# Optimization experiments

Hardware: AMD Instinct MI355X
Metric: run time of the kernel (lower is better)

## Reference

```python
import jax, jax.numpy as jnp
import numpy as np

N_ENT = 100000
N_REL = 200  # directed relations = 2*N_REL
DIM = 200
N_EDGE = 1000000


def rotate(h, r):
    # complex 'rotate' composition: split last dim into (real, imag) halves
    d = h.shape[-1] // 2
    h_re, h_im = h[..., :d], h[..., d:]
    r_re, r_im = r[..., :d], r[..., d:]
    return jnp.concatenate([h_re * r_re - h_im * r_im,
                            h_re * r_im + h_im * r_re], axis=-1)


def setup_inputs() -> dict:
    key = jax.random.key(0)
    ks = jax.random.split(key, 8)
    return {
        "ent_emb": jax.random.normal(ks[0], (N_ENT, DIM), jnp.float32),
        "rel_emb": jax.random.normal(ks[1], (2 * N_REL, DIM), jnp.float32),
        "loop_rel": jax.random.normal(ks[2], (1, DIM), jnp.float32),
        "w_in": jax.random.normal(ks[3], (DIM, DIM), jnp.float32) * (DIM ** -0.5),
        "w_out": jax.random.normal(ks[4], (DIM, DIM), jnp.float32) * (DIM ** -0.5),
        "w_loop": jax.random.normal(ks[5], (DIM, DIM), jnp.float32) * (DIM ** -0.5),
        "bias": jnp.zeros((DIM,), jnp.float32),
        "bn_gamma": jnp.ones((DIM,), jnp.float32),
        "bn_beta": jnp.zeros((DIM,), jnp.float32),
        "edge_index": jax.random.randint(ks[6], (2, N_EDGE), 0, N_ENT, jnp.int64 if jax.config.jax_enable_x64 else jnp.int32),
        "edge_type": jax.random.randint(ks[7], (N_EDGE,), 0, N_REL, jnp.int64 if jax.config.jax_enable_x64 else jnp.int32),
    }


def reference(ent_emb, rel_emb, loop_rel, w_in, w_out, w_loop, bias,
              bn_gamma, bn_beta, edge_index, edge_type):
    n = ent_emb.shape[0]
    num_rel = rel_emb.shape[0] // 2
    src, dst = edge_index[0], edge_index[1]

    def direction(s, d, etype, W):
        # gather -> compose -> transform: [E, DIM]
        msg = rotate(ent_emb[s], rel_emb[etype]) @ W
        # symmetric degree normalization (CompGCN compute_norm)
        deg = jax.ops.segment_sum(jnp.ones_like(s, ent_emb.dtype), d, num_segments=n)
        inv = jnp.where(deg > 0, deg ** -0.5, 0.0)
        norm = inv[d] * inv[s]
        return jax.ops.segment_sum(msg * norm[:, None], d, num_segments=n)

    in_res = direction(src, dst, edge_type, w_in)
    out_res = direction(dst, src, edge_type + num_rel, w_out)  # inverse edges
    loop_res = rotate(ent_emb, loop_rel) @ w_loop

    out = (in_res + out_res + loop_res) * (1.0 / 3.0) + bias
    # BatchNorm1d over entities (training-mode batch stats)
    mean = out.mean(axis=0)
    var = out.var(axis=0)
    out = (out - mean) * jax.lax.rsqrt(var + 1e-5) * bn_gamma + bn_beta
    return jnp.tanh(out)
```

## Files before the change

### kernel.cpp

```cpp
#include <hip/hip_runtime.h>
#include <math.h>
#include <stdint.h>

#define N_ENT   100000
#define DIM     200
#define HD      100
#define N_RELC  200
#define KP      608
#define BM      128
#define BNN     256
#define NT      19
#define MPAD    100096
#define SCAN_B  2048
#define SCAN_NB 49

typedef uint32_t u32;
typedef __attribute__((ext_vector_type(8))) short bf16x8;
typedef __attribute__((ext_vector_type(4))) float f32x4;

__device__ __forceinline__ float invsqrt_pos(float x) {
    return x > 0.f ? (1.f / sqrtf(x)) : 0.f;
}

__device__ __forceinline__ u32 pack_bf16x2(float a, float b) {
    u32 ua = __float_as_uint(a), ub = __float_as_uint(b);
    ua = (ua + 0x7FFFu + ((ua >> 16) & 1u)) >> 16;
    ub = (ub + 0x7FFFu + ((ub >> 16) & 1u)) >> 16;
    return ua | (ub << 16);
}

__device__ __forceinline__ float bf_lo(u32 u) { return __uint_as_float(u << 16); }
__device__ __forceinline__ float bf_hi(u32 u) { return __uint_as_float(u & 0xFFFF0000u); }

__device__ __forceinline__ void lds_cp16(void* lds, const void* g) {
    auto gp = (const __attribute__((address_space(1))) u32*)(uintptr_t)g;
    auto lp = (__attribute__((address_space(3))) u32*)(u32)(uintptr_t)lds;
    __builtin_amdgcn_global_load_lds(gp, lp, 16, 0, 0);
}

__global__ __launch_bounds__(256) void conv_ent_kernel(
        const float* __restrict__ ent, const float* __restrict__ loop_rel,
        ushort* __restrict__ ent16, ushort* __restrict__ Abuf) {
    int row  = (blockIdx.x * blockDim.x + threadIdx.x) >> 6;
    int lane = threadIdx.x & 63;
    if (row >= N_ENT) return;
    u32* Arow = (u32*)(Abuf + (size_t)row * KP);
    if (lane < 50) {
        const float* h = ent + (size_t)row * DIM;
        float2 re = *(const float2*)(h + 2 * lane);
        float2 im = *(const float2*)(h + HD + 2 * lane);
        u32* e32 = (u32*)(ent16 + (size_t)row * DIM);
        e32[lane]      = pack_bf16x2(re.x, re.y);
        e32[50 + lane] = pack_bf16x2(im.x, im.y);
        float2 lre = *(const float2*)(loop_rel + 2 * lane);
        float2 lim = *(const float2*)(loop_rel + HD + 2 * lane);
        float rx = re.x * lre.x - im.x * lim.x;
        float ry = re.y * lre.y - im.y * lim.y;
        float ix = re.x * lim.x + im.x * lre.x;
        float iy = re.y * lim.y + im.y * lre.y;
        Arow[200 + lane] = pack_bf16x2(rx, ry);
        Arow[250 + lane] = pack_bf16x2(ix, iy);
    } else if (lane < 54) {
        Arow[300 + (lane - 50)] = 0u;
    }
}

__global__ __launch_bounds__(256) void conv_rel_kernel(
        const float* __restrict__ src, ushort* __restrict__ dst, int n4) {
    int i = blockIdx.x * blockDim.x + threadIdx.x;
    int stride = gridDim.x * blockDim.x;
    for (; i < n4; i += stride) {
        float4 v = ((const float4*)src)[i];
        uint2 o;
        o.x = pack_bf16x2(v.x, v.y);
        o.y = pack_bf16x2(v.z, v.w);
        ((uint2*)dst)[i] = o;
    }
}

__global__ __launch_bounds__(256) void deg_kernel(
        const int* __restrict__ src, const int* __restrict__ dst,
        int* __restrict__ deg_in, int* __restrict__ deg_out, int n) {
    int i = blockIdx.x * blockDim.x + threadIdx.x;
    int stride = gridDim.x * blockDim.x;
    for (; i < n; i += stride) {
        atomicAdd(&deg_in[dst[i]], 1);
        atomicAdd(&deg_out[src[i]], 1);
    }
}

__global__ __launch_bounds__(256) void scan_part_kernel(
        const int* __restrict__ deg_in, const int* __restrict__ deg_out,
        int* __restrict__ partials) {
    int dir = blockIdx.x >= SCAN_NB;
    int blk = blockIdx.x - dir * SCAN_NB;
    const int* deg = dir ? deg_out : deg_in;
    int t = threadIdx.x;
    int base = blk * SCAN_B + t * 8;
    int s = 0;
#pragma unroll
    for (int u = 0; u < 8; ++u) {
        int i = base + u;
        if (i < N_ENT) s += deg[i];
    }
    __shared__ int red[256];
    red[t] = s;
    __syncthreads();
    for (int d = 128; d > 0; d >>= 1) {
        if (t < d) red[t] += red[t + d];
        __syncthreads();
    }
    if (t == 0) partials[dir * SCAN_NB + blk] = red[0];
}

__global__ __launch_bounds__(256) void scan_apply_kernel(
        const int* __restrict__ deg_in, const int* __restrict__ deg_out,
        const int* __restrict__ partials,
        int* __restrict__ off_in, int* __restrict__ off_out,
        int* __restrict__ cur_in, int* __restrict__ cur_out,
        float* __restrict__ inv_in, float* __restrict__ inv_out) {
    int dir = blockIdx.x >= SCAN_NB;
    int blk = blockIdx.x - dir * SCAN_NB;
    const int* deg = dir ? deg_out : deg_in;
    int* off   = dir ? off_out : off_in;
    int* cur   = dir ? cur_out : cur_in;
    float* inv = dir ? inv_out : inv_in;
    int t = threadIdx.x;
    int base = blk * SCAN_B + t * 8;
    int v[8];
    int s = 0;
#pragma unroll
    for (int u = 0; u < 8; ++u) {
        int i = base + u;
        v[u] = (i < N_ENT) ? deg[i] : 0;
        s += v[u];
    }
    __shared__ int red[256];
    red[t] = s;
    __syncthreads();
    for (int d = 1; d < 256; d <<= 1) {
        int x = (t >= d) ? red[t - d] : 0;
        __syncthreads();
        red[t] += x;
        __syncthreads();
    }
    int base_off = 0;
    for (int b = 0; b < blk; ++b) base_off += partials[dir * SCAN_NB + b];
    int run = base_off + red[t] - s;
#pragma unroll
    for (int u = 0; u < 8; ++u) {
        int i = base + u;
        if (i < N_ENT) {
            off[i] = run;
            cur[i] = run;
            inv[i] = invsqrt_pos((float)v[u]);
            run += v[u];
            if (i == N_ENT - 1) off[N_ENT] = run;
        }
    }
}

__global__ __launch_bounds__(256) void fill_kernel(
        const int* __restrict__ src, const int* __restrict__ dst,
        const int* __restrict__ etype,
        int* cur_in, int* cur_out,
        u32* __restrict__ csr_in, u32* __restrict__ csr_out, int n) {
    int tid  = blockIdx.x * blockDim.x + threadIdx.x;
    int nthr = gridDim.x * blockDim.x;
    for (int base = tid; base < n; base += 4 * nthr) {
        int i0 = base;
        int i1 = base + nthr;
        int i2 = base + 2 * nthr;
        int i3 = base + 3 * nthr;
        bool k1 = i1 < n, k2 = i2 < n, k3 = i3 < n;
        int s0 = src[i0], d0 = dst[i0], e0 = etype[i0];
        int s1 = 0, d1 = 0, e1 = 0, s2 = 0, d2 = 0, e2 = 0, s3 = 0, d3 = 0, e3 = 0;
        if (k1) { s1 = src[i1]; d1 = dst[i1]; e1 = etype[i1]; }
        if (k2) { s2 = src[i2]; d2 = dst[i2]; e2 = etype[i2]; }
        if (k3) { s3 = src[i3]; d3 = dst[i3]; e3 = etype[i3]; }
        int pi0 = atomicAdd(&cur_in[d0], 1);
        int po0 = atomicAdd(&cur_out[s0], 1);
        int pi1 = 0, po1 = 0, pi2 = 0, po2 = 0, pi3 = 0, po3 = 0;
        if (k1) { pi1 = atomicAdd(&cur_in[d1], 1); po1 = atomicAdd(&cur_out[s1], 1); }
        if (k2) { pi2 = atomicAdd(&cur_in[d2], 1); po2 = atomicAdd(&cur_out[s2], 1); }
        if (k3) { pi3 = atomicAdd(&cur_in[d3], 1); po3 = atomicAdd(&cur_out[s3], 1); }
        csr_in[pi0]  = ((u32)s0 << 8) | (u32)e0;
        csr_out[po0] = ((u32)d0 << 8) | (u32)e0;
        if (k1) { csr_in[pi1]  = ((u32)s1 << 8) | (u32)e1;
                  csr_out[po1] = ((u32)d1 << 8) | (u32)e1; }
        if (k2) { csr_in[pi2]  = ((u32)s2 << 8) | (u32)e2;
                  csr_out[po2] = ((u32)d2 << 8) | (u32)e2; }
        if (k3) { csr_in[pi3]  = ((u32)s3 << 8) | (u32)e3;
                  csr_out[po3] = ((u32)d3 << 8) | (u32)e3; }
    }
}

__global__ __launch_bounds__(256) void prep_bt_kernel(
        const float* __restrict__ w_in, const float* __restrict__ w_out,
        const float* __restrict__ w_loop, ushort* __restrict__ BT) {
    int i = blockIdx.x * 256 + threadIdx.x;
    if (i >= 256 * KP) return;
    int c = i / KP, k = i % KP;
    float v = 0.f;
    if (c < DIM) {
        if (k < 200)      v = w_in[k * DIM + c];
        else if (k < 400) v = w_out[(k - 200) * DIM + c];
        else if (k < 600) v = w_loop[(k - 400) * DIM + c];
    }
    u32 u = __float_as_uint(v);
    u = (u + 0x7FFFu + ((u >> 16) & 1u)) >> 16;
    BT[i] = (ushort)u;
}

__global__ __launch_bounds__(256) void gather_kernel(
        const ushort* __restrict__ ent16, const ushort* __restrict__ rel16,
        const u32* __restrict__ csr_in, const u32* __restrict__ csr_out,
        const int* __restrict__ off_in, const int* __restrict__ off_out,
        const float* __restrict__ inv_in, const float* __restrict__ inv_out,
        ushort* __restrict__ Abuf) {
    int node = (blockIdx.x * blockDim.x + threadIdx.x) >> 6;
    int lane = threadIdx.x & 63;
    if (node >= N_ENT) return;
    const bool act = lane < 50;
    u32* Arow = (u32*)(Abuf + (size_t)node * KP);

#pragma unroll
    for (int dir = 0; dir < 2; ++dir) {
        const u32* csr = dir ? csr_out : csr_in;
        const int* off = dir ? off_out : off_in;
        const float* inv = dir ? inv_out : inv_in;
        const int tofs = dir ? N_RELC : 0;
        float myinv = inv[node];
        float2 are = {0.f, 0.f}, aim = {0.f, 0.f};
        float2 bre = {0.f, 0.f}, bim = {0.f, 0.f};
        float2 cre = {0.f, 0.f}, cim = {0.f, 0.f};
        float2 dre = {0.f, 0.f}, dim_ = {0.f, 0.f};
        int i0 = off[node], i1 = off[node + 1];
        int i = i0;
        for (; i + 3 < i1; i += 4) {
            u32 pk0 = csr[i],     pk1 = csr[i + 1];
            u32 pk2 = csr[i + 2], pk3 = csr[i + 3];
            int s0 = (int)(pk0 >> 8), t0 = (int)(pk0 & 255u) + tofs;
            int s1 = (int)(pk1 >> 8), t1 = (int)(pk1 & 255u) + tofs;
            int s2 = (int)(pk2 >> 8), t2 = (int)(pk2 & 255u) + tofs;
            int s3 = (int)(pk3 >> 8), t3 = (int)(pk3 & 255u) + tofs;
            float n0 = myinv * inv[s0];
            float n1 = myinv * inv[s1];
            float n2 = myinv * inv[s2];
            float n3 = myinv * inv[s3];
            if (act) {
                const u32* h0 = (const u32*)(ent16 + (size_t)s0 * DIM);
                const u32* r0 = (const u32*)(rel16 + (size_t)t0 * DIM);
                const u32* h1 = (const u32*)(ent16 + (size_t)s1 * DIM);
                const u32* r1 = (const u32*)(rel16 + (size_t)t1 * DIM);
                const u32* h2 = (const u32*)(ent16 + (size_t)s2 * DIM);
                const u32* r2 = (const u32*)(rel16 + (size_t)t2 * DIM);
                const u32* h3 = (const u32*)(ent16 + (size_t)s3 * DIM);
                const u32* r3 = (const u32*)(rel16 + (size_t)t3 * DIM);
                u32 hre0 = h0[lane], him0 = h0[50 + lane];
                u32 rre0 = r0[lane], rim0 = r0[50 + lane];
                u32 hre1 = h1[lane], him1 = h1[50 + lane];
                u32 rre1 = r1[lane], rim1 = r1[50 + lane];
                u32 hre2 = h2[lane], him2 = h2[50 + lane];
                u32 rre2 = r2[lane], rim2 = r2[50 + lane];
                u32 hre3 = h3[lane], him3 = h3[50 + lane];
                u32 rre3 = r3[lane], rim3 = r3[50 + lane];
                {
                    float ha = bf_lo(hre0), hb = bf_hi(hre0);
                    float ia = bf_lo(him0), ib = bf_hi(him0);
                    float ra = bf_lo(rre0), rb = bf_hi(rre0);
                    float ja = bf_lo(rim0), jb = bf_hi(rim0);
                    are.x += (ha * ra - ia * ja) * n0;
                    are.y += (hb * rb - ib * jb) * n0;
                    aim.x += (ha * ja + ia * ra) * n0;
                    aim.y += (hb * jb + ib * rb) * n0;
                }
                {
                    float ha = bf_lo(hre1), hb = bf_hi(hre1);
                    float ia = bf_lo(him1), ib = bf_hi(him1);
                    float ra = bf_lo(rre1), rb = bf_hi(rre1);
                    float ja = bf_lo(rim1), jb = bf_hi(rim1);
                    bre.x += (ha * ra - ia * ja) * n1;
                    bre.y += (hb * rb - ib * jb) * n1;
                    bim.x += (ha * ja + ia * ra) * n1;
                    bim.y += (hb * jb + ib * rb) * n1;
                }
                {
                    float ha = bf_lo(hre2), hb = bf_hi(hre2);
                    float ia = bf_lo(him2), ib = bf_hi(him2);
                    float ra = bf_lo(rre2), rb = bf_hi(rre2);
                    float ja = bf_lo(rim2), jb = bf_hi(rim2);
                    cre.x += (ha * ra - ia * ja) * n2;
                    cre.y += (hb * rb - ib * jb) * n2;
                    cim.x += (ha * ja + ia * ra) * n2;
                    cim.y += (hb * jb + ib * rb) * n2;
                }
                {
                    float ha = bf_lo(hre3), hb = bf_hi(hre3);
                    float ia = bf_lo(him3), ib = bf_hi(him3);
                    float ra = bf_lo(rre3), rb = bf_hi(rre3);
                    float ja = bf_lo(rim3), jb = bf_hi(rim3);
                    dre.x += (ha * ra - ia * ja) * n3;
                    dre.y += (hb * rb - ib * jb) * n3;
                    dim_.x += (ha * ja + ia * ra) * n3;
                    dim_.y += (hb * jb + ib * rb) * n3;
                }
            }
        }
        for (; i < i1; ++i) {
            u32 pk = csr[i];
            int s = (int)(pk >> 8), t = (int)(pk & 255u) + tofs;
            float nrm = myinv * inv[s];
            if (act) {
                const u32* h32 = (const u32*)(ent16 + (size_t)s * DIM);
                const u32* r32 = (const u32*)(rel16 + (size_t)t * DIM);
                u32 hre = h32[lane], him = h32[50 + lane];
                u32 rre = r32[lane], rim = r32[50 + lane];
                float ha = bf_lo(hre), hb = bf_hi(hre);
                float ia = bf_lo(him), ib = bf_hi(him);
                float ra = bf_lo(rre), rb = bf_hi(rre);
                float ja = bf_lo(rim), jb = bf_hi(rim);
                are.x += (ha * ra - ia * ja) * nrm;
                are.y += (hb * rb - ib * jb) * nrm;
                aim.x += (ha * ja + ia * ra) * nrm;
                aim.y += (hb * jb + ib * rb) * nrm;
            }
        }
        if (act) {
            are.x += bre.x + cre.x + dre.x;
            are.y += bre.y + cre.y + dre.y;
            aim.x += bim.x + cim.x + dim_.x;
            aim.y += bim.y + cim.y + dim_.y;
            Arow[dir * 100 + lane]      = pack_bf16x2(are.x, are.y);
            Arow[dir * 100 + 50 + lane] = pack_bf16x2(aim.x, aim.y);
        }
    }
}

__global__ __launch_bounds__(512, 4) void gemm_kernel(
        const ushort* __restrict__ A, const ushort* __restrict__ BT,
        const float* __restrict__ bias, float* __restrict__ out,
        float* __restrict__ stats) {
    __shared__ ushort Asm[2][BM * 32];
    __shared__ ushort Bsm[2][BNN * 32];
    __shared__ float sredS[8][4][16];
    __shared__ float sredQ[8][4][16];
    const int tid = threadIdx.x;
    const int row0 = blockIdx.x * BM;
    const int l = tid & 63;
    const int w = tid >> 6;
    const int wm = w >> 2;
    const int wn = w & 3;

    f32x4 acc[4][4];
#pragma unroll
    for (int i = 0; i < 4; ++i)
#pragma unroll
        for (int j = 0; j < 4; ++j)
            acc[i][j] = (f32x4){0.f, 0.f, 0.f, 0.f};

    {
        int r = tid >> 2, s = tid & 3;
        lds_cp16(&Asm[0][tid * 8], A + (size_t)(row0 + r) * KP + s * 8);
#pragma unroll
        for (int j = 0; j < 2; ++j) {
            int c = tid + j * 512;
            int br = c >> 2, bs = c & 3;
            lds_cp16(&Bsm[0][c * 8], BT + (size_t)br * KP + bs * 8);
        }
    }

    int cur = 0;
    for (int ks = 0; ks < NT; ++ks) {
        __syncthreads();
        if (ks + 1 < NT) {
            const int k0 = (ks + 1) * 32;
            int r = tid >> 2, s = tid & 3;
            lds_cp16(&Asm[cur ^ 1][tid * 8], A + (size_t)(row0 + r) * KP + k0 + s * 8);
#pragma unroll
            for (int j = 0; j < 2; ++j) {
                int c = tid + j * 512;
                int br = c >> 2, bs = c & 3;
                lds_cp16(&Bsm[cur ^ 1][c * 8], BT + (size_t)br * KP + k0 + bs * 8);
            }
        }
        const int kq = (l >> 4) * 8;
        const int lr = l & 15;
        bf16x8 aF[4], bF[4];
#pragma unroll
        for (int mf = 0; mf < 4; ++mf)
            aF[mf] = *(const bf16x8*)&Asm[cur][(wm * 64 + mf * 16 + lr) * 32 + kq];
#pragma unroll
        for (int nf = 0; nf < 4; ++nf)
            bF[nf] = *(const bf16x8*)&Bsm[cur][(wn * 64 + nf * 16 + lr) * 32 + kq];
#pragma unroll
        for (int mf = 0; mf < 4; ++mf)
#pragma unroll
            for (int nf = 0; nf < 4; ++nf)
                acc[mf][nf] = __builtin_amdgcn_mfma_f32_16x16x32_bf16(
                        aF[mf], bF[nf], acc[mf][nf], 0, 0, 0);
        cur ^= 1;
    }

    const int lr = l & 15;
    const int rq = (l >> 4) * 4;
    float colS[4], colQ[4];
#pragma unroll
    for (int nf = 0; nf < 4; ++nf) { colS[nf] = 0.f; colQ[nf] = 0.f; }

#pragma unroll
    for (int nf = 0; nf < 4; ++nf) {
        int gcol = wn * 64 + nf * 16 + lr;
        bool cok = gcol < DIM;
        float b = cok ? bias[gcol] : 0.f;
#pragma unroll
        for (int mf = 0; mf < 4; ++mf) {
            int grow0 = row0 + wm * 64 + mf * 16 + rq;
#pragma unroll
            for (int r = 0; r < 4; ++r) {
                int grow = grow0 + r;
                if (grow < N_ENT && cok) {
                    float v = acc[mf][nf][r] * (1.f / 3.f) + b;
                    out[(size_t)grow * DIM + gcol] = v;
                    colS[nf] += v;
                    colQ[nf] += v * v;
                }
            }
        }
    }
#pragma unroll
    for (int nf = 0; nf < 4; ++nf) {
        colS[nf] += __shfl_down(colS[nf], 32);
        colS[nf] += __shfl_down(colS[nf], 16);
        colQ[nf] += __shfl_down(colQ[nf], 32);
        colQ[nf] += __shfl_down(colQ[nf], 16);
    }
    if (l < 16) {
#pragma unroll
        for (int nf = 0; nf < 4; ++nf) {
            sredS[w][nf][l] = colS[nf];
            sredQ[w][nf][l] = colQ[nf];
        }
    }
    __syncthreads();
    if (tid < DIM) {
        int wn_ = tid >> 6, nf_ = (tid >> 4) & 3, lr_ = tid & 15;
        float s = sredS[wn_][nf_][lr_] + sredS[wn_ + 4][nf_][lr_];
        float q = sredQ[wn_][nf_][lr_] + sredQ[wn_ + 4][nf_][lr_];
        atomicAdd(&stats[tid], s);
        atomicAdd(&stats[DIM + tid], q);
    }
}

__global__ __launch_bounds__(256) void bn_tanh_kernel(
        float* __restrict__ out, const float* __restrict__ stats,
        const float* __restrict__ gamma, const float* __restrict__ beta) {
    __shared__ float ssc[DIM], ssh[DIM];
    int t = threadIdx.x;
    if (t < DIM) {
        float mean = stats[t] * (1.f / (float)N_ENT);
        float var  = stats[DIM + t] * (1.f / (float)N_ENT) - mean * mean;
        float scale = gamma[t] / sqrtf(var + 1e-5f);
        ssc[t] = scale;
        ssh[t] = beta[t] - mean * scale;
    }
    __syncthreads();
    size_t i = (size_t)blockIdx.x * blockDim.x + threadIdx.x;
    size_t stride = (size_t)gridDim.x * blockDim.x;
    const size_t n4 = (size_t)N_ENT * DIM / 4;
    float4* p = (float4*)out;
    for (; i < n4; i += stride) {
        int c = (int)((i * 4) % DIM);
        float4 v = p[i];
        v.x = tanhf(v.x * ssc[c]     + ssh[c]);
        v.y = tanhf(v.y * ssc[c + 1] + ssh[c + 1]);
        v.z = tanhf(v.z * ssc[c + 2] + ssh[c + 2]);
        v.w = tanhf(v.w * ssc[c + 3] + ssh[c + 3]);
        p[i] = v;
    }
}

extern "C" void kernel_launch(void* const* d_in, const int* in_sizes, int n_in,
                              void* d_out, int out_size, void* d_ws, size_t ws_size,
                              hipStream_t stream) {
    const float* ent      = (const float*)d_in[0];
    const float* rel      = (const float*)d_in[1];
    const float* loop_rel = (const float*)d_in[2];
    const float* w_in     = (const float*)d_in[3];
    const float* w_out    = (const float*)d_in[4];
    const float* w_loop   = (const float*)d_in[5];
    const float* bias     = (const float*)d_in[6];
    const float* gamma    = (const float*)d_in[7];
    const float* beta     = (const float*)d_in[8];
    const int*   eidx     = (const int*)d_in[9];
    const int*   etype    = (const int*)d_in[10];
    const int n_edge = in_sizes[10];
    const int* src = eidx;
    const int* dst = eidx + n_edge;

    ushort* Abuf   = (ushort*)d_ws;
    ushort* BT     = Abuf + (size_t)MPAD * KP;
    int* deg_in    = (int*)(BT + 256 * KP);
    int* deg_out   = deg_in + N_ENT;
    int* off_in    = deg_out + N_ENT;
    int* off_out   = off_in + N_ENT + 1;
    int* cur_in    = off_out + N_ENT + 1;
    int* cur_out   = cur_in + N_ENT;
    float* inv_in  = (float*)(cur_out + N_ENT);
    float* inv_out = inv_in + N_ENT;
    int* partials  = (int*)(inv_out + N_ENT);
    u32* csr_in    = (u32*)(partials + 2 * SCAN_NB);
    u32* csr_out   = csr_in + n_edge;
    float* stats   = (float*)(csr_out + n_edge);
    ushort* rel16  = (ushort*)(stats + 2 * DIM);
    float* outp    = (float*)d_out;
    ushort* ent16  = (ushort*)d_out;

    hipMemsetAsync(deg_in, 0, (size_t)2 * N_ENT * sizeof(int), stream);
    hipMemsetAsync(stats, 0, (size_t)2 * DIM * sizeof(float), stream);

    conv_ent_kernel<<<(N_ENT * 64 + 255) / 256, 256, 0, stream>>>(
        ent, loop_rel, ent16, Abuf);
    conv_rel_kernel<<<79, 256, 0, stream>>>(rel, rel16, 2 * N_RELC * DIM / 4);
    deg_kernel<<<2048, 256, 0, stream>>>(src, dst, deg_in, deg_out, n_edge);
    scan_part_kernel<<<2 * SCAN_NB, 256, 0, stream>>>(deg_in, deg_out, partials);
    scan_apply_kernel<<<2 * SCAN_NB, 256, 0, stream>>>(
        deg_in, deg_out, partials, off_in, off_out, cur_in, cur_out,
        inv_in, inv_out);
    fill_kernel<<<512, 256, 0, stream>>>(src, dst, etype, cur_in, cur_out,
                                         csr_in, csr_out, n_edge);
    prep_bt_kernel<<<(256 * KP + 255) / 256, 256, 0, stream>>>(w_in, w_out, w_loop, BT);
    gather_kernel<<<25000, 256, 0, stream>>>(ent16, rel16, csr_in, csr_out,
                                             off_in, off_out, inv_in, inv_out, Abuf);
    gemm_kernel<<<MPAD / BM, 512, 0, stream>>>(Abuf, BT, bias, outp, stats);
    bn_tanh_kernel<<<2048, 256, 0, stream>>>(outp, stats, gamma, beta);
}
```

Baseline: 537.8 us.

## Fuse prep kernels and use fp16 dot2 interleaved complex layout in gather

Merges the entity conversion, relation conversion, weight transpose and degree-count kernels into one launch partitioned by block index, which cuts launch overhead and lets the independent stages overlap. The gather stage now stores entity embeddings as interleaved fp16 (re,im) pairs and precomputes two relation variants, (re,-im) and (im,re), so each complex product becomes one v_dot2 instruction per component instead of several bf16 unpacks and FMAs. Each edge now reads three 8-byte vectors, and fp16 has a narrower range than bf16, which changes precision.

```diff
diff --git a/kernel.cpp b/kernel.cpp
--- a/kernel.cpp
+++ b/kernel.cpp
@@ -14,9 +14,15 @@
 #define SCAN_B  2048
 #define SCAN_NB 49
 
+#define CE_B    25000
+#define CR_B    100
+#define PB_B    608
+#define DEG_B   1024
+
 typedef uint32_t u32;
 typedef __attribute__((ext_vector_type(8))) short bf16x8;
 typedef __attribute__((ext_vector_type(4))) float f32x4;
+typedef _Float16 h16x2 __attribute__((ext_vector_type(2)));
 
 __device__ __forceinline__ float invsqrt_pos(float x) {
     return x > 0.f ? (1.f / sqrtf(x)) : 0.f;
@@ -29,8 +35,17 @@
     return ua | (ub << 16);
 }
 
-__device__ __forceinline__ float bf_lo(u32 u) { return __uint_as_float(u << 16); }
-__device__ __forceinline__ float bf_hi(u32 u) { return __uint_as_float(u & 0xFFFF0000u); }
+__device__ __forceinline__ u32 pack_h2(float a, float b) {
+    _Float16 ha = (_Float16)a, hb = (_Float16)b;
+    ushort ua = __builtin_bit_cast(ushort, ha);
+    ushort ub = __builtin_bit_cast(ushort, hb);
+    return (u32)ua | ((u32)ub << 16);
+}
+
+__device__ __forceinline__ float dot2h(u32 a, u32 b, float c) {
+    return __builtin_amdgcn_fdot2(__builtin_bit_cast(h16x2, a),
+                                  __builtin_bit_cast(h16x2, b), c, false);
+}
 
 __device__ __forceinline__ void lds_cp16(void* lds, const void* g) {
     auto gp = (const __attribute__((address_space(1))) u32*)(uintptr_t)g;
@@ -38,54 +53,74 @@
     __builtin_amdgcn_global_load_lds(gp, lp, 16, 0, 0);
 }
 
-__global__ __launch_bounds__(256) void conv_ent_kernel(
-        const float* __restrict__ ent, const float* __restrict__ loop_rel,
-        ushort* __restrict__ ent16, ushort* __restrict__ Abuf) {
-    int row  = (blockIdx.x * blockDim.x + threadIdx.x) >> 6;
-    int lane = threadIdx.x & 63;
-    if (row >= N_ENT) return;
-    u32* Arow = (u32*)(Abuf + (size_t)row * KP);
-    if (lane < 50) {
-        const float* h = ent + (size_t)row * DIM;
-        float2 re = *(const float2*)(h + 2 * lane);
-        float2 im = *(const float2*)(h + HD + 2 * lane);
-        u32* e32 = (u32*)(ent16 + (size_t)row * DIM);
-        e32[lane]      = pack_bf16x2(re.x, re.y);
-        e32[50 + lane] = pack_bf16x2(im.x, im.y);
-        float2 lre = *(const float2*)(loop_rel + 2 * lane);
-        float2 lim = *(const float2*)(loop_rel + HD + 2 * lane);
-        float rx = re.x * lre.x - im.x * lim.x;
-        float ry = re.y * lre.y - im.y * lim.y;
-        float ix = re.x * lim.x + im.x * lre.x;
-        float iy = re.y * lim.y + im.y * lre.y;
-        Arow[200 + lane] = pack_bf16x2(rx, ry);
-        Arow[250 + lane] = pack_bf16x2(ix, iy);
-    } else if (lane < 54) {
-        Arow[300 + (lane - 50)] = 0u;
-    }
-}
-
-__global__ __launch_bounds__(256) void conv_rel_kernel(
-        const float* __restrict__ src, ushort* __restrict__ dst, int n4) {
-    int i = blockIdx.x * blockDim.x + threadIdx.x;
-    int stride = gridDim.x * blockDim.x;
-    for (; i < n4; i += stride) {
-        float4 v = ((const float4*)src)[i];
-        uint2 o;
-        o.x = pack_bf16x2(v.x, v.y);
-        o.y = pack_bf16x2(v.z, v.w);
-        ((uint2*)dst)[i] = o;
-    }
-}
-
-__global__ __launch_bounds__(256) void deg_kernel(
+__global__ __launch_bounds__(256) void prep_kernel(
+        const float* __restrict__ ent, const float* __restrict__ rel,
+        const float* __restrict__ loop_rel,
+        const float* __restrict__ w_in, const float* __restrict__ w_out,
+        const float* __restrict__ w_loop,
         const int* __restrict__ src, const int* __restrict__ dst,
-        int* __restrict__ deg_in, int* __restrict__ deg_out, int n) {
-    int i = blockIdx.x * blockDim.x + threadIdx.x;
-    int stride = gridDim.x * blockDim.x;
-    for (; i < n; i += stride) {
-        atomicAdd(&deg_in[dst[i]], 1);
-        atomicAdd(&deg_out[src[i]], 1);
+        u32* __restrict__ ent16h, u32* __restrict__ relng,
+        u32* __restrict__ relsw, ushort* __restrict__ BT,
+        ushort* __restrict__ Abuf,
+        int* __restrict__ deg_in, int* __restrict__ deg_out, int n_edge) {
+    const int b = blockIdx.x;
+    const int tid = threadIdx.x;
+    if (b < CE_B) {
+        int row  = (b * 256 + tid) >> 6;
+        int lane = tid & 63;
+        if (row >= N_ENT) return;
+        u32* Arow = (u32*)(Abuf + (size_t)row * KP);
+        if (lane < 50) {
+            const float* h = ent + (size_t)row * DIM;
+            float2 re = *(const float2*)(h + 2 * lane);
+            float2 im = *(const float2*)(h + HD + 2 * lane);
+            uint2 o;
+            o.x = pack_h2(re.x, im.x);
+            o.y = pack_h2(re.y, im.y);
+            ((uint2*)(ent16h + (size_t)row * 100))[lane] = o;
+            float2 lre = *(const float2*)(loop_rel + 2 * lane);
+            float2 lim = *(const float2*)(loop_rel + HD + 2 * lane);
+            float rx = re.x * lre.x - im.x * lim.x;
+            float ry = re.y * lre.y - im.y * lim.y;
+            float ix = re.x * lim.x + im.x * lre.x;
+            float iy = re.y * lim.y + im.y * lre.y;
+            Arow[200 + lane] = pack_bf16x2(rx, ry);
+            Arow[250 + lane] = pack_bf16x2(ix, iy);
+        } else if (lane < 54) {
+            Arow[300 + (lane - 50)] = 0u;
+        }
+    } else if (b < CE_B + CR_B) {
+        int row  = ((b - CE_B) * 256 + tid) >> 6;
+        int lane = tid & 63;
+        if (row >= 2 * N_RELC || lane >= 50) return;
+        const float* r = rel + (size_t)row * DIM;
+        float2 re = *(const float2*)(r + 2 * lane);
+        float2 im = *(const float2*)(r + HD + 2 * lane);
+        uint2 g, w;
+        g.x = pack_h2(re.x, -im.x); g.y = pack_h2(re.y, -im.y);
+        w.x = pack_h2(im.x, re.x);  w.y = pack_h2(im.y, re.y);
+        ((uint2*)(relng + (size_t)row * 100))[lane] = g;
+        ((uint2*)(relsw + (size_t)row * 100))[lane] = w;
+    } else if (b < CE_B + CR_B + PB_B) {
+        int i = (b - CE_B - CR_B) * 256 + tid;
+        if (i >= 256 * KP) return;
+        int c = i / KP, k = i % KP;
+        float v = 0.f;
+        if (c < DIM) {
+            if (k < 200)      v = w_in[k * DIM + c];
+            else if (k < 400) v = w_out[(k - 200) * DIM + c];
+            else if (k < 600) v = w_loop[(k - 400) * DIM + c];
+        }
+        u32 u = __float_as_uint(v);
+        u = (u + 0x7FFFu + ((u >> 16) & 1u)) >> 16;
+        BT[i] = (ushort)u;
+    } else {
+        int i = (b - CE_B - CR_B - PB_B) * 256 + tid;
+        int stride = DEG_B * 256;
+        for (; i < n_edge; i += stride) {
+            atomicAdd(&deg_in[dst[i]], 1);
+            atomicAdd(&deg_out[src[i]], 1);
+        }
     }
 }
 
@@ -145,7 +180,7 @@
         __syncthreads();
     }
     int base_off = 0;
-    for (int b = 0; b < blk; ++b) base_off += partials[dir * SCAN_NB + b];
+    for (int bq = 0; bq < blk; ++bq) base_off += partials[dir * SCAN_NB + bq];
     int run = base_off + red[t] - s;
 #pragma unroll
     for (int u = 0; u < 8; ++u) {
@@ -195,25 +230,9 @@
     }
 }
 
-__global__ __launch_bounds__(256) void prep_bt_kernel(
-        const float* __restrict__ w_in, const float* __restrict__ w_out,
-        const float* __restrict__ w_loop, ushort* __restrict__ BT) {
-    int i = blockIdx.x * 256 + threadIdx.x;
-    if (i >= 256 * KP) return;
-    int c = i / KP, k = i % KP;
-    float v = 0.f;
-    if (c < DIM) {
-        if (k < 200)      v = w_in[k * DIM + c];
-        else if (k < 400) v = w_out[(k - 200) * DIM + c];
-        else if (k < 600) v = w_loop[(k - 400) * DIM + c];
-    }
-    u32 u = __float_as_uint(v);
-    u = (u + 0x7FFFu + ((u >> 16) & 1u)) >> 16;
-    BT[i] = (ushort)u;
-}
-
 __global__ __launch_bounds__(256) void gather_kernel(
-        const ushort* __restrict__ ent16, const ushort* __restrict__ rel16,
+        const u32* __restrict__ ent16h,
+        const u32* __restrict__ relng, const u32* __restrict__ relsw,
         const u32* __restrict__ csr_in, const u32* __restrict__ csr_out,
         const int* __restrict__ off_in, const int* __restrict__ off_out,
         const float* __restrict__ inv_in, const float* __restrict__ inv_out,
@@ -221,6 +240,7 @@
     int node = (blockIdx.x * blockDim.x + threadIdx.x) >> 6;
     int lane = threadIdx.x & 63;
     if (node >= N_ENT) return;
+    const int ll = lane < 50 ? lane : 49;
     const bool act = lane < 50;
     u32* Arow = (u32*)(Abuf + (size_t)node * KP);
 
@@ -249,62 +269,34 @@
             float n2 = myinv * inv[s2];
             float n3 = myinv * inv[s3];
             if (act) {
-                const u32* h0 = (const u32*)(ent16 + (size_t)s0 * DIM);
-                const u32* r0 = (const u32*)(rel16 + (size_t)t0 * DIM);
-                const u32* h1 = (const u32*)(ent16 + (size_t)s1 * DIM);
-                const u32* r1 = (const u32*)(rel16 + (size_t)t1 * DIM);
-                const u32* h2 = (const u32*)(ent16 + (size_t)s2 * DIM);
-                const u32* r2 = (const u32*)(rel16 + (size_t)t2 * DIM);
-                const u32* h3 = (const u32*)(ent16 + (size_t)s3 * DIM);
-                const u32* r3 = (const u32*)(rel16 + (size_t)t3 * DIM);
-                u32 hre0 = h0[lane], him0 = h0[50 + lane];
-                u32 rre0 = r0[lane], rim0 = r0[50 + lane];
-                u32 hre1 = h1[lane], him1 = h1[50 + lane];
-                u32 rre1 = r1[lane], rim1 = r1[50 + lane];
-                u32 hre2 = h2[lane], him2 = h2[50 + lane];
-                u32 rre2 = r2[lane], rim2 = r2[50 + lane];
-                u32 hre3 = h3[lane], him3 = h3[50 + lane];
-                u32 rre3 = r3[lane], rim3 = r3[50 + lane];
-                {
-                    float ha = bf_lo(hre0), hb = bf_hi(hre0);
-                    float ia = bf_lo(him0), ib = bf_hi(him0);
-                    float ra = bf_lo(rre0), rb = bf_hi(rre0);
-                    float ja = bf_lo(rim0), jb = bf_hi(rim0);
-                    are.x += (ha * ra - ia * ja) * n0;
-                    are.y += (hb * rb - ib * jb) * n0;
-                    aim.x += (ha * ja + ia * ra) * n0;
-                    aim.y += (hb * jb + ib * rb) * n0;
-                }
-                {
-                    float ha = bf_lo(hre1), hb = bf_hi(hre1);
-                    float ia = bf_lo(him1), ib = bf_hi(him1);
-                    float ra = bf_lo(rre1), rb = bf_hi(rre1);
-                    float ja = bf_lo(rim1), jb = bf_hi(rim1);
-                    bre.x += (ha * ra - ia * ja) * n1;
-                    bre.y += (hb * rb - ib * jb) * n1;
-                    bim.x += (ha * ja + ia * ra) * n1;
-                    bim.y += (hb * jb + ib * rb) * n1;
-                }
-                {
-                    float ha = bf_lo(hre2), hb = bf_hi(hre2);
-                    float ia = bf_lo(him2), ib = bf_hi(him2);
-                    float ra = bf_lo(rre2), rb = bf_hi(rre2);
-                    float ja = bf_lo(rim2), jb = bf_hi(rim2);
-                    cre.x += (ha * ra - ia * ja) * n2;
-                    cre.y += (hb * rb - ib * jb) * n2;
-                    cim.x += (ha * ja + ia * ra) * n2;
-                    cim.y += (hb * jb + ib * rb) * n2;
-                }
-                {
-                    float ha = bf_lo(hre3), hb = bf_hi(hre3);
-                    float ia = bf_lo(him3), ib = bf_hi(him3);
-                    float ra = bf_lo(rre3), rb = bf_hi(rre3);
-                    float ja = bf_lo(rim3), jb = bf_hi(rim3);
-                    dre.x += (ha * ra - ia * ja) * n3;
-                    dre.y += (hb * rb - ib * jb) * n3;
-                    dim_.x += (ha * ja + ia * ra) * n3;
-                    dim_.y += (hb * jb + ib * rb) * n3;
-                }
+                uint2 hv0 = ((const uint2*)(ent16h + (size_t)s0 * 100))[ll];
+                uint2 gv0 = ((const uint2*)(relng  + (size_t)t0 * 100))[ll];
+                uint2 wv0 = ((const uint2*)(relsw  + (size_t)t0 * 100))[ll];
+                uint2 hv1 = ((const uint2*)(ent16h + (size_t)s1 * 100))[ll];
+                uint2 gv1 = ((const uint2*)(relng  + (size_t)t1 * 100))[ll];
+                uint2 wv1 = ((const uint2*)(relsw  + (size_t)t1 * 100))[ll];
+                uint2 hv2 = ((const uint2*)(ent16h + (size_t)s2 * 100))[ll];
+                uint2 gv2 = ((const uint2*)(relng  + (size_t)t2 * 100))[ll];
+                uint2 wv2 = ((const uint2*)(relsw  + (size_t)t2 * 100))[ll];
+                uint2 hv3 = ((const uint2*)(ent16h + (size_t)s3 * 100))[ll];
+                uint2 gv3 = ((const uint2*)(relng  + (size_t)t3 * 100))[ll];
+                uint2 wv3 = ((const uint2*)(relsw  + (size_t)t3 * 100))[ll];
+                are.x  = fmaf(dot2h(hv0.x, gv0.x, 0.f), n0, are.x);
+                are.y  = fmaf(dot2h(hv0.y, gv0.y, 0.f), n0, are.y);
+                aim.x  = fmaf(dot2h(hv0.x, wv0.x, 0.f), n0, aim.x);
+                aim.y  = fmaf(dot2h(hv0.y, wv0.y, 0.f), n0, aim.y);
+                bre.x  = fmaf(dot2h(hv1.x, gv1.x, 0.f), n1, bre.x);
+                bre.y  = fmaf(dot2h(hv1.y, gv1.y, 0.f), n1, bre.y);
+                bim.x  = fmaf(dot2h(hv1.x, wv1.x, 0.f), n1, bim.x);
+                bim.y  = fmaf(dot2h(hv1.y, wv1.y, 0.f), n1, bim.y);
+                cre.x  = fmaf(dot2h(hv2.x, gv2.x, 0.f), n2, cre.x);
+                cre.y  = fmaf(dot2h(hv2.y, gv2.y, 0.f), n2, cre.y);
+                cim.x  = fmaf(dot2h(hv2.x, wv2.x, 0.f), n2, cim.x);
+                cim.y  = fmaf(dot2h(hv2.y, wv2.y, 0.f), n2, cim.y);
+                dre.x  = fmaf(dot2h(hv3.x, gv3.x, 0.f), n3, dre.x);
+                dre.y  = fmaf(dot2h(hv3.y, gv3.y, 0.f), n3, dre.y);
+                dim_.x = fmaf(dot2h(hv3.x, wv3.x, 0.f), n3, dim_.x);
+                dim_.y = fmaf(dot2h(hv3.y, wv3.y, 0.f), n3, dim_.y);
             }
         }
         for (; i < i1; ++i) {
@@ -312,18 +304,13 @@
             int s = (int)(pk >> 8), t = (int)(pk & 255u) + tofs;
             float nrm = myinv * inv[s];
             if (act) {
-                const u32* h32 = (const u32*)(ent16 + (size_t)s * DIM);
-                const u32* r32 = (const u32*)(rel16 + (size_t)t * DIM);
-                u32 hre = h32[lane], him = h32[50 + lane];
-                u32 rre = r32[lane], rim = r32[50 + lane];
-                float ha = bf_lo(hre), hb = bf_hi(hre);
-                float ia = bf_lo(him), ib = bf_hi(him);
-                float ra = bf_lo(rre), rb = bf_hi(rre);
-                float ja = bf_lo(rim), jb = bf_hi(rim);
-                are.x += (ha * ra - ia * ja) * nrm;
-                are.y += (hb * rb - ib * jb) * nrm;
-                aim.x += (ha * ja + ia * ra) * nrm;
-                aim.y += (hb * jb + ib * rb) * nrm;
+                uint2 hv = ((const uint2*)(ent16h + (size_t)s * 100))[ll];
+                uint2 gv = ((const uint2*)(relng  + (size_t)t * 100))[ll];
+                uint2 wv = ((const uint2*)(relsw  + (size_t)t * 100))[ll];
+                are.x = fmaf(dot2h(hv.x, gv.x, 0.f), nrm, are.x);
+                are.y = fmaf(dot2h(hv.y, gv.y, 0.f), nrm, are.y);
+                aim.x = fmaf(dot2h(hv.x, wv.x, 0.f), nrm, aim.x);
+                aim.y = fmaf(dot2h(hv.y, wv.y, 0.f), nrm, aim.y);
             }
         }
         if (act) {
@@ -512,26 +499,26 @@
     u32* csr_in    = (u32*)(partials + 2 * SCAN_NB);
     u32* csr_out   = csr_in + n_edge;
     float* stats   = (float*)(csr_out + n_edge);
-    ushort* rel16  = (ushort*)(stats + 2 * DIM);
+    u32* relng     = (u32*)(stats + 2 * DIM);
+    u32* relsw     = relng + 2 * N_RELC * 100;
     float* outp    = (float*)d_out;
-    ushort* ent16  = (ushort*)d_out;
+    u32* ent16h    = (u32*)d_out;
 
     hipMemsetAsync(deg_in, 0, (size_t)2 * N_ENT * sizeof(int), stream);
     hipMemsetAsync(stats, 0, (size_t)2 * DIM * sizeof(float), stream);
 
-    conv_ent_kernel<<<(N_ENT * 64 + 255) / 256, 256, 0, stream>>>(
-        ent, loop_rel, ent16, Abuf);
-    conv_rel_kernel<<<79, 256, 0, stream>>>(rel, rel16, 2 * N_RELC * DIM / 4);
-    deg_kernel<<<2048, 256, 0, stream>>>(src, dst, deg_in, deg_out, n_edge);
+    prep_kernel<<<CE_B + CR_B + PB_B + DEG_B, 256, 0, stream>>>(
+        ent, rel, loop_rel, w_in, w_out, w_loop, src, dst,
+        ent16h, relng, relsw, BT, Abuf, deg_in, deg_out, n_edge);
     scan_part_kernel<<<2 * SCAN_NB, 256, 0, stream>>>(deg_in, deg_out, partials);
     scan_apply_kernel<<<2 * SCAN_NB, 256, 0, stream>>>(
         deg_in, deg_out, partials, off_in, off_out, cur_in, cur_out,
         inv_in, inv_out);
     fill_kernel<<<512, 256, 0, stream>>>(src, dst, etype, cur_in, cur_out,
                                          csr_in, csr_out, n_edge);
-    prep_bt_kernel<<<(256 * KP + 255) / 256, 256, 0, stream>>>(w_in, w_out, w_loop, BT);
-    gather_kernel<<<25000, 256, 0, stream>>>(ent16, rel16, csr_in, csr_out,
-                                             off_in, off_out, inv_in, inv_out, Abuf);
+    gather_kernel<<<25000, 256, 0, stream>>>(ent16h, relng, relsw,
+                                             csr_in, csr_out, off_in, off_out,
+                                             inv_in, inv_out, Abuf);
     gemm_kernel<<<MPAD / BM, 512, 0, stream>>>(Abuf, BT, bias, outp, stats);
     bn_tanh_kernel<<<2048, 256, 0, stream>>>(outp, stats, gamma, beta);
 }
```

New measurement: 587.4 us. 1.09x slower.
